# Kernel optimization log

Hardware: AMD Instinct MI355X
Metric: run time of the kernel (lower is better)

## Reference

```python
import jax, jax.numpy as jnp
import numpy as np

N_HEADS = 18
HEAD_DIM = 16
ROPE_THETA = 10000.0
SLIDING_WINDOW = 4096


def _rotate_half(x):
    half = x.shape[-1] // 2
    return jnp.concatenate([-x[..., half:], x[..., :half]], axis=-1)


def setup_inputs() -> dict:
    key = jax.random.key(0)
    k0, k1, k2, k3, k4 = jax.random.split(key, 5)
    B, S, H = 2, 2048, 288
    std = 0.02
    return {
        "hidden_states": jax.random.normal(k0, (B, S, H), dtype=jnp.float32),
        "Wq": jax.random.normal(k1, (H, H), dtype=jnp.float32) * std,
        "Wk": jax.random.normal(k2, (H, H), dtype=jnp.float32) * std,
        "Wv": jax.random.normal(k3, (H, H), dtype=jnp.float32) * std,
        "Wo": jax.random.normal(k4, (H, H), dtype=jnp.float32) * std,
    }


def reference(hidden_states, Wq, Wk, Wv, Wo):
    B, S, H = hidden_states.shape
    nH, D = N_HEADS, HEAD_DIM

    # QKV projections (nn.Linear: y = x @ W.T), reshape to [B, nH, S, D]
    def proj(W):
        return jnp.einsum("bsh,oh->bso", hidden_states, W).reshape(B, S, nH, D).transpose(0, 2, 1, 3)

    q, k, v = proj(Wq), proj(Wk), proj(Wv)

    # Rotary embedding: position_ids = arange(S)
    pos = jnp.arange(S, dtype=jnp.float32)
    inv_freq = 1.0 / (ROPE_THETA ** (jnp.arange(0, D, 2, dtype=jnp.float32) / D))
    freqs = pos[:, None] * inv_freq[None, :]            # [S, D/2]
    emb = jnp.concatenate([freqs, freqs], axis=-1)      # [S, D]
    cos = jnp.cos(emb)[None, None, :, :]                # [1, 1, S, D]
    sin = jnp.sin(emb)[None, None, :, :]
    q = q * cos + _rotate_half(q) * sin
    k = k * cos + _rotate_half(k) * sin

    # num_key_value_groups = 1 -> repeat_kv is identity.
    scores = jnp.einsum("bhqd,bhkd->bhqk", q, k) / jnp.sqrt(jnp.float32(D))

    # Sliding-window causal mask: attend iff 0 <= i - j < window
    i = jnp.arange(S)[:, None]
    j = jnp.arange(S)[None, :]
    allowed = (j <= i) & (i - j < SLIDING_WINDOW)       # [S, S]
    neg = jnp.finfo(scores.dtype).min
    scores = jnp.where(allowed[None, None, :, :], scores, neg)

    attn = jax.nn.softmax(scores.astype(jnp.float32), axis=-1).astype(q.dtype)
    out = jnp.einsum("bhqk,bhkd->bhqd", attn, v)        # [B, nH, S, D]
    out = out.transpose(0, 2, 1, 3).reshape(B, S, H)
    return jnp.einsum("bsh,oh->bso", out, Wo)
```

## Files before the change

kernel.cpp:

```cpp
#include <hip/hip_runtime.h>
#include <hip/hip_bf16.h>
#include <math.h>

#define H_DIM 288
#define NHEADS 18
#define HEAD_D 16
#define SEQ 2048
#define BATCH 2
#define M_TOT (BATCH*SEQ)
#define XCNT (M_TOT*H_DIM)
#define WCNT (H_DIM*H_DIM)
#define NUNITS 10368
#define NQUNITS 2304

typedef _Float16 f16_t;
typedef __attribute__((ext_vector_type(4))) _Float16 half4v;
typedef __attribute__((ext_vector_type(8))) _Float16 half8v;
typedef __attribute__((ext_vector_type(4))) float   float4v;

__global__ __launch_bounds__(256) void cvt_f16(
    const float* __restrict__ X,
    const float* __restrict__ Wq, const float* __restrict__ Wk,
    const float* __restrict__ Wv, const float* __restrict__ Wo,
    f16_t* __restrict__ Xf, f16_t* __restrict__ Wf)
{
    int idx = blockIdx.x * 256 + threadIdx.x;
    const int X4 = XCNT/4, W4 = WCNT/4;
    if (idx >= X4 + 4*W4) return;
    const float* src; f16_t* dst; int off;
    if (idx < X4) { src = X; dst = Xf; off = idx; }
    else {
        int r = idx - X4;
        int wz = r / W4; off = r - wz*W4;
        src = (wz==0) ? Wq : (wz==1) ? Wk : (wz==2) ? Wv : Wo;
        dst = Wf + (size_t)wz*WCNT;
    }
    float4 v = ((const float4*)src)[off];
    half4v h; h[0]=(f16_t)v.x; h[1]=(f16_t)v.y; h[2]=(f16_t)v.z; h[3]=(f16_t)v.w;
    ((half4v*)dst)[off] = h;
}

__global__ __launch_bounds__(64) void qkv_mfma(
    const f16_t* __restrict__ Xf, const f16_t* __restrict__ Wf,
    f16_t* __restrict__ Q16, f16_t* __restrict__ K16, f16_t* __restrict__ Vt)
{
    const int bx = blockIdx.x;
    const int z  = bx/6;
    const int n0 = (bx - z*6)*48;
    const int m0 = blockIdx.y*32;
    const int lane = threadIdx.x & 63;
    const int n = lane & 15, quad = lane >> 4;

    const f16_t* W = Wf + (size_t)z*WCNT;

    float4v acc[2][3];
    #pragma unroll
    for (int mt = 0; mt < 2; mt++)
        #pragma unroll
        for (int nt = 0; nt < 3; nt++)
            acc[mt][nt] = (float4v){0.f,0.f,0.f,0.f};

    for (int k0 = 0; k0 < H_DIM; k0 += 32) {
        half8v a[2], b[3];
        #pragma unroll
        for (int mt = 0; mt < 2; mt++)
            a[mt] = *(const half8v*)(Xf + (size_t)(m0 + mt*16 + n)*H_DIM + k0 + quad*8);
        #pragma unroll
        for (int nt = 0; nt < 3; nt++)
            b[nt] = *(const half8v*)(W + (size_t)(n0 + nt*16 + n)*H_DIM + k0 + quad*8);
        #pragma unroll
        for (int mt = 0; mt < 2; mt++)
            #pragma unroll
            for (int nt = 0; nt < 3; nt++)
                acc[mt][nt] = __builtin_amdgcn_mfma_f32_16x16x32_f16(a[mt], b[nt], acc[mt][nt], 0, 0, 0);
    }

    if (z < 2) {
        f16_t* dst = (z == 0) ? Q16 : K16;
        const float invf = exp2f(-1.6609640474436813f * (float)(n & 7));
        #pragma unroll
        for (int mt = 0; mt < 2; mt++) {
            #pragma unroll
            for (int r = 0; r < 4; r++) {
                int m = m0 + mt*16 + quad*4 + r;
                int bb = m >> 11, s = m & (SEQ - 1);
                float ang = (float)s * invf;
                float c, sn;
                sincosf(ang, &sn, &c);
                #pragma unroll
                for (int nt = 0; nt < 3; nt++) {
                    float own = acc[mt][nt][r];
                    float par = __shfl_xor(own, 8, 64);
                    float val = (n & 8) ? fmaf(own, c, par*sn) : fmaf(own, c, -par*sn);
                    if (z == 0) val *= 0.36067376022224085f;
                    int head = (n0 >> 4) + nt;
                    dst[((size_t)((bb*NHEADS + head)*SEQ) + s)*HEAD_D + n] = (f16_t)val;
                }
            }
        }
    } else {
        #pragma unroll
        for (int mt = 0; mt < 2; mt++)
            #pragma unroll
            for (int nt = 0; nt < 3; nt++)
                #pragma unroll
                for (int r = 0; r < 4; r++) {
                    int m = m0 + mt*16 + quad*4 + r;
                    int bb = m >> 11, s = m & (SEQ - 1);
                    int head = (n0 >> 4) + nt;
                    Vt[(size_t)(bb*NHEADS + head)*(SEQ*HEAD_D)
                       + (size_t)(s >> 4)*256 + n*16 + (s & 15)] = (f16_t)acc[mt][nt][r];
                }
    }
}

__global__ __launch_bounds__(256) void attn_part(
    const f16_t* __restrict__ Q16, const f16_t* __restrict__ K16,
    const f16_t* __restrict__ Vt,
    float4* __restrict__ accbuf, float* __restrict__ lbuf)
{
    const int unit = blockIdx.x*4 + (threadIdx.x >> 6);
    const int lane = threadIdx.x & 63;
    const int n = lane & 15, quad = lane >> 4;

    const int bh = unit / 288;
    const int rem = unit - bh*288;
    int g, t0;
    if      (rem < 8)   { g=0; t0=rem;     }
    else if (rem < 24)  { g=1; t0=rem-8;   }
    else if (rem < 48)  { g=2; t0=rem-24;  }
    else if (rem < 80)  { g=3; t0=rem-48;  }
    else if (rem < 120) { g=4; t0=rem-80;  }
    else if (rem < 168) { g=5; t0=rem-120; }
    else if (rem < 224) { g=6; t0=rem-168; }
    else                { g=7; t0=rem-224; }
    const int qd = t0 / (g+1);
    const int qp = 8*g + qd;
    const int chunk = t0 - qd*(g+1);
    const int q0 = qp*32;

    half4v qb0 = *(const half4v*)(Q16 + ((size_t)bh*SEQ + q0 + n)*HEAD_D + quad*4);
    half4v qb1 = *(const half4v*)(Q16 + ((size_t)bh*SEQ + q0 + 16 + n)*HEAD_D + quad*4);
    const f16_t* Kb = K16 + (size_t)bh * SEQ * HEAD_D;
    const f16_t* Vb = Vt  + (size_t)bh * SEQ * HEAD_D;

    const float4v zero = {0.f, 0.f, 0.f, 0.f};
    float4v acc0 = zero, acc1 = zero;
    float l0 = 0.f, l1 = 0.f;

    const int lim0 = 2*qp, lim1 = 2*qp + 1;
    const int ktlo = chunk*16;
    const int kthi = min(ktlo + 15, lim1);

    int kt = ktlo;
    half4v ka = *(const half4v*)(Kb + (size_t)(kt*16 + n)*HEAD_D + quad*4);
    half4v va = *(const half4v*)(Vb + (size_t)kt*256 + n*16 + quad*4);
    for (; kt <= kthi; kt++) {
        half4v kan, van;
        if (kt < kthi) {
            kan = *(const half4v*)(Kb + (size_t)((kt+1)*16 + n)*HEAD_D + quad*4);
            van = *(const half4v*)(Vb + (size_t)(kt+1)*256 + n*16 + quad*4);
        }
        {
            float4v s = __builtin_amdgcn_mfma_f32_16x16x16f16(ka, qb1, zero, 0, 0, 0);
            float p[4];
            #pragma unroll
            for (int r = 0; r < 4; r++) {
                float e = __builtin_amdgcn_exp2f(s[r]);
                p[r] = (kt == lim1 && quad*4 + r > n) ? 0.0f : e;
            }
            l1 += (p[0] + p[1]) + (p[2] + p[3]);
            half4v pb;
            pb[0]=(f16_t)p[0]; pb[1]=(f16_t)p[1]; pb[2]=(f16_t)p[2]; pb[3]=(f16_t)p[3];
            acc1 = __builtin_amdgcn_mfma_f32_16x16x16f16(va, pb, acc1, 0, 0, 0);
        }
        if (kt <= lim0) {
            float4v s = __builtin_amdgcn_mfma_f32_16x16x16f16(ka, qb0, zero, 0, 0, 0);
            float p[4];
            #pragma unroll
            for (int r = 0; r < 4; r++) {
                float e = __builtin_amdgcn_exp2f(s[r]);
                p[r] = (kt == lim0 && quad*4 + r > n) ? 0.0f : e;
            }
            l0 += (p[0] + p[1]) + (p[2] + p[3]);
            half4v pb;
            pb[0]=(f16_t)p[0]; pb[1]=(f16_t)p[1]; pb[2]=(f16_t)p[2]; pb[3]=(f16_t)p[3];
            acc0 = __builtin_amdgcn_mfma_f32_16x16x16f16(va, pb, acc0, 0, 0, 0);
        }
        ka = kan; va = van;
    }

    float4 a0; a0.x=acc0[0]; a0.y=acc0[1]; a0.z=acc0[2]; a0.w=acc0[3];
    float4 a1; a1.x=acc1[0]; a1.y=acc1[1]; a1.z=acc1[2]; a1.w=acc1[3];
    accbuf[((size_t)unit*2 + 0)*64 + lane] = a0;
    accbuf[((size_t)unit*2 + 1)*64 + lane] = a1;
    lbuf[((size_t)unit*2 + 0)*64 + lane] = l0;
    lbuf[((size_t)unit*2 + 1)*64 + lane] = l1;
}

__global__ __launch_bounds__(256) void attn_red(
    const float4* __restrict__ accbuf, const float* __restrict__ lbuf,
    f16_t* __restrict__ Of)
{
    const int wid = blockIdx.x*4 + (threadIdx.x >> 6);
    const int lane = threadIdx.x & 63;
    const int n = lane & 15, quad = lane >> 4;
    const int bh = wid >> 6, qp = wid & 63;
    const int b = bh / NHEADS, h = bh - b*NHEADS;
    const int g = qp >> 3, j = qp & 7;
    const int nch = g + 1;
    const int ubase = bh*288 + qp + 4*g*(g-1) + g*j;

    #pragma unroll
    for (int t = 0; t < 2; t++) {
        float4 a = {0.f, 0.f, 0.f, 0.f};
        float l = 0.f;
        for (int c = 0; c < nch; c++) {
            size_t idx = ((size_t)(ubase + c)*2 + t)*64 + lane;
            float4 v = accbuf[idx];
            a.x += v.x; a.y += v.y; a.z += v.z; a.w += v.w;
            l += lbuf[idx];
        }
        l += __shfl_xor(l, 16, 64);
        l += __shfl_xor(l, 32, 64);
        float inv = 1.0f / l;
        half4v o;
        o[0]=(f16_t)(a.x*inv); o[1]=(f16_t)(a.y*inv);
        o[2]=(f16_t)(a.z*inv); o[3]=(f16_t)(a.w*inv);
        *(half4v*)(Of + (size_t)(b*SEQ + qp*32 + t*16 + n)*H_DIM + h*HEAD_D + quad*4) = o;
    }
}

__global__ __launch_bounds__(64) void out_mfma(
    const f16_t* __restrict__ Of, const f16_t* __restrict__ Wo16,
    float* __restrict__ C)
{
    const int n0 = blockIdx.x * 48;
    const int m0 = blockIdx.y * 32;
    const int lane = threadIdx.x & 63;
    const int n = lane & 15, quad = lane >> 4;

    float4v acc[2][3];
    #pragma unroll
    for (int mt = 0; mt < 2; mt++)
        #pragma unroll
        for (int nt = 0; nt < 3; nt++)
            acc[mt][nt] = (float4v){0.f,0.f,0.f,0.f};

    for (int k0 = 0; k0 < H_DIM; k0 += 32) {
        half8v a[2], b[3];
        #pragma unroll
        for (int mt = 0; mt < 2; mt++)
            a[mt] = *(const half8v*)(Of + (size_t)(m0 + mt*16 + n)*H_DIM + k0 + quad*8);
        #pragma unroll
        for (int nt = 0; nt < 3; nt++)
            b[nt] = *(const half8v*)(Wo16 + (size_t)(n0 + nt*16 + n)*H_DIM + k0 + quad*8);
        #pragma unroll
        for (int mt = 0; mt < 2; mt++)
            #pragma unroll
            for (int nt = 0; nt < 3; nt++)
                acc[mt][nt] = __builtin_amdgcn_mfma_f32_16x16x32_f16(a[mt], b[nt], acc[mt][nt], 0, 0, 0);
    }
    #pragma unroll
    for (int mt = 0; mt < 2; mt++)
        #pragma unroll
        for (int nt = 0; nt < 3; nt++)
            #pragma unroll
            for (int r = 0; r < 4; r++) {
                int m = m0 + mt*16 + quad*4 + r;
                C[(size_t)m*H_DIM + n0 + nt*16 + n] = acc[mt][nt][r];
            }
}

extern "C" void kernel_launch(void* const* d_in, const int* in_sizes, int n_in,
                              void* d_out, int out_size, void* d_ws, size_t ws_size,
                              hipStream_t stream)
{
    const float* Xh = (const float*)d_in[0];
    const float* Wq = (const float*)d_in[1];
    const float* Wk = (const float*)d_in[2];
    const float* Wv = (const float*)d_in[3];
    const float* Wo = (const float*)d_in[4];
    float* out = (float*)d_out;

    f16_t* Xf  = (f16_t*)d_ws;
    f16_t* Wf  = Xf + XCNT;
    f16_t* Q16 = Wf + 4*(size_t)WCNT;
    f16_t* K16 = Q16 + XCNT;
    f16_t* Vt  = K16 + XCNT;
    f16_t* Of  = Vt + XCNT;
    float4* accbuf = (float4*)(Of + XCNT);
    float*  lbuf   = (float*)(accbuf + (size_t)NUNITS*2*64);

    const int total4 = (XCNT + 4*WCNT)/4;
    cvt_f16<<<dim3((total4 + 255)/256), 256, 0, stream>>>(Xh, Wq, Wk, Wv, Wo, Xf, Wf);
    qkv_mfma<<<dim3(18, 128), 64, 0, stream>>>(Xf, Wf, Q16, K16, Vt);
    attn_part<<<dim3(NUNITS/4), 256, 0, stream>>>(Q16, K16, Vt, accbuf, lbuf);
    attn_red<<<dim3(NQUNITS/4), 256, 0, stream>>>(accbuf, lbuf, Of);
    out_mfma<<<dim3(6, 128), 64, 0, stream>>>(Of, Wf + 3*(size_t)WCNT, out);
}
```

Before: 116.6 us.

## Fuse all five stages into one cooperative persistent kernel with grid syncs

Replaces the five separate launches (convert, QKV GEMM, partial attention, reduction, output GEMM) with a single cooperative kernel of 512 blocks that loops over each stage's work units and separates stages with grid.sync(). This is meant to remove per-launch overhead and inter-kernel gaps. It also adds a fully unrolled fast path for unmasked 16-tile attention chunks that preloads all K/V fragments before computing. In exchange it relies on cooperative launch residency, adds grid-wide barrier cost, and raises register pressure under launch_bounds(256,2).

```diff
diff --git a/kernel.cpp b/kernel.cpp
--- a/kernel.cpp
+++ b/kernel.cpp
@@ -1,6 +1,9 @@
 #include <hip/hip_runtime.h>
 #include <hip/hip_bf16.h>
+#include <hip/hip_cooperative_groups.h>
 #include <math.h>
+
+namespace cg = cooperative_groups;
 
 #define H_DIM 288
 #define NHEADS 18
@@ -12,264 +15,287 @@
 #define WCNT (H_DIM*H_DIM)
 #define NUNITS 10368
 #define NQUNITS 2304
+#define NBLK 512
+#define NGW (NBLK*4)
 
 typedef _Float16 f16_t;
 typedef __attribute__((ext_vector_type(4))) _Float16 half4v;
 typedef __attribute__((ext_vector_type(8))) _Float16 half8v;
 typedef __attribute__((ext_vector_type(4))) float   float4v;
 
-__global__ __launch_bounds__(256) void cvt_f16(
+__global__ __launch_bounds__(256, 2) void fused_attn(
     const float* __restrict__ X,
     const float* __restrict__ Wq, const float* __restrict__ Wk,
     const float* __restrict__ Wv, const float* __restrict__ Wo,
-    f16_t* __restrict__ Xf, f16_t* __restrict__ Wf)
+    float* __restrict__ out,
+    f16_t* __restrict__ Xf, f16_t* __restrict__ Wf,
+    f16_t* __restrict__ Q16, f16_t* __restrict__ K16, f16_t* __restrict__ Vt,
+    f16_t* __restrict__ Of, float4* __restrict__ accbuf, float* __restrict__ lbuf)
 {
-    int idx = blockIdx.x * 256 + threadIdx.x;
-    const int X4 = XCNT/4, W4 = WCNT/4;
-    if (idx >= X4 + 4*W4) return;
-    const float* src; f16_t* dst; int off;
-    if (idx < X4) { src = X; dst = Xf; off = idx; }
-    else {
-        int r = idx - X4;
-        int wz = r / W4; off = r - wz*W4;
-        src = (wz==0) ? Wq : (wz==1) ? Wk : (wz==2) ? Wv : Wo;
-        dst = Wf + (size_t)wz*WCNT;
-    }
-    float4 v = ((const float4*)src)[off];
-    half4v h; h[0]=(f16_t)v.x; h[1]=(f16_t)v.y; h[2]=(f16_t)v.z; h[3]=(f16_t)v.w;
-    ((half4v*)dst)[off] = h;
-}
-
-__global__ __launch_bounds__(64) void qkv_mfma(
-    const f16_t* __restrict__ Xf, const f16_t* __restrict__ Wf,
-    f16_t* __restrict__ Q16, f16_t* __restrict__ K16, f16_t* __restrict__ Vt)
-{
-    const int bx = blockIdx.x;
-    const int z  = bx/6;
-    const int n0 = (bx - z*6)*48;
-    const int m0 = blockIdx.y*32;
+    cg::grid_group grid = cg::this_grid();
+    const int wave = threadIdx.x >> 6;
     const int lane = threadIdx.x & 63;
     const int n = lane & 15, quad = lane >> 4;
-
-    const f16_t* W = Wf + (size_t)z*WCNT;
-
-    float4v acc[2][3];
-    #pragma unroll
-    for (int mt = 0; mt < 2; mt++)
-        #pragma unroll
-        for (int nt = 0; nt < 3; nt++)
-            acc[mt][nt] = (float4v){0.f,0.f,0.f,0.f};
-
-    for (int k0 = 0; k0 < H_DIM; k0 += 32) {
-        half8v a[2], b[3];
+    const int gwave = blockIdx.x*4 + wave;
+
+    {
+        const int tid = blockIdx.x*256 + threadIdx.x;
+        const int X4 = XCNT/4, W4 = WCNT/4;
+        const int total4 = X4 + 4*W4;
+        for (int i = tid; i < total4; i += NBLK*256) {
+            const float* src; f16_t* dst; int off;
+            if (i < X4) { src = X; dst = Xf; off = i; }
+            else {
+                int r = i - X4;
+                int wz = r / W4; off = r - wz*W4;
+                src = (wz==0) ? Wq : (wz==1) ? Wk : (wz==2) ? Wv : Wo;
+                dst = Wf + (size_t)wz*WCNT;
+            }
+            float4 v = ((const float4*)src)[off];
+            half4v h; h[0]=(f16_t)v.x; h[1]=(f16_t)v.y; h[2]=(f16_t)v.z; h[3]=(f16_t)v.w;
+            ((half4v*)dst)[off] = h;
+        }
+    }
+    grid.sync();
+
+    for (int u = gwave; u < 2304; u += NGW) {
+        const int bx = u % 18;
+        const int by = u / 18;
+        const int z  = bx/6;
+        const int n0 = (bx - z*6)*48;
+        const int m0 = by*32;
+        const f16_t* W = Wf + (size_t)z*WCNT;
+
+        float4v acc[2][3];
         #pragma unroll
         for (int mt = 0; mt < 2; mt++)
-            a[mt] = *(const half8v*)(Xf + (size_t)(m0 + mt*16 + n)*H_DIM + k0 + quad*8);
-        #pragma unroll
-        for (int nt = 0; nt < 3; nt++)
-            b[nt] = *(const half8v*)(W + (size_t)(n0 + nt*16 + n)*H_DIM + k0 + quad*8);
-        #pragma unroll
-        for (int mt = 0; mt < 2; mt++)
-            #pragma unroll
-            for (int nt = 0; nt < 3; nt++)
-                acc[mt][nt] = __builtin_amdgcn_mfma_f32_16x16x32_f16(a[mt], b[nt], acc[mt][nt], 0, 0, 0);
-    }
-
-    if (z < 2) {
-        f16_t* dst = (z == 0) ? Q16 : K16;
-        const float invf = exp2f(-1.6609640474436813f * (float)(n & 7));
-        #pragma unroll
-        for (int mt = 0; mt < 2; mt++) {
-            #pragma unroll
-            for (int r = 0; r < 4; r++) {
-                int m = m0 + mt*16 + quad*4 + r;
-                int bb = m >> 11, s = m & (SEQ - 1);
-                float ang = (float)s * invf;
-                float c, sn;
-                sincosf(ang, &sn, &c);
-                #pragma unroll
-                for (int nt = 0; nt < 3; nt++) {
-                    float own = acc[mt][nt][r];
-                    float par = __shfl_xor(own, 8, 64);
-                    float val = (n & 8) ? fmaf(own, c, par*sn) : fmaf(own, c, -par*sn);
-                    if (z == 0) val *= 0.36067376022224085f;
-                    int head = (n0 >> 4) + nt;
-                    dst[((size_t)((bb*NHEADS + head)*SEQ) + s)*HEAD_D + n] = (f16_t)val;
-                }
-            }
-        }
-    } else {
-        #pragma unroll
-        for (int mt = 0; mt < 2; mt++)
-            #pragma unroll
-            for (int nt = 0; nt < 3; nt++)
+            #pragma unroll
+            for (int nt = 0; nt < 3; nt++)
+                acc[mt][nt] = (float4v){0.f,0.f,0.f,0.f};
+
+        for (int k0 = 0; k0 < H_DIM; k0 += 32) {
+            half8v a[2], b[3];
+            #pragma unroll
+            for (int mt = 0; mt < 2; mt++)
+                a[mt] = *(const half8v*)(Xf + (size_t)(m0 + mt*16 + n)*H_DIM + k0 + quad*8);
+            #pragma unroll
+            for (int nt = 0; nt < 3; nt++)
+                b[nt] = *(const half8v*)(W + (size_t)(n0 + nt*16 + n)*H_DIM + k0 + quad*8);
+            #pragma unroll
+            for (int mt = 0; mt < 2; mt++)
+                #pragma unroll
+                for (int nt = 0; nt < 3; nt++)
+                    acc[mt][nt] = __builtin_amdgcn_mfma_f32_16x16x32_f16(a[mt], b[nt], acc[mt][nt], 0, 0, 0);
+        }
+
+        if (z < 2) {
+            f16_t* dst = (z == 0) ? Q16 : K16;
+            const float invf = exp2f(-1.6609640474436813f * (float)(n & 7));
+            #pragma unroll
+            for (int mt = 0; mt < 2; mt++) {
                 #pragma unroll
                 for (int r = 0; r < 4; r++) {
                     int m = m0 + mt*16 + quad*4 + r;
                     int bb = m >> 11, s = m & (SEQ - 1);
-                    int head = (n0 >> 4) + nt;
-                    Vt[(size_t)(bb*NHEADS + head)*(SEQ*HEAD_D)
-                       + (size_t)(s >> 4)*256 + n*16 + (s & 15)] = (f16_t)acc[mt][nt][r];
-                }
-    }
-}
-
-__global__ __launch_bounds__(256) void attn_part(
-    const f16_t* __restrict__ Q16, const f16_t* __restrict__ K16,
-    const f16_t* __restrict__ Vt,
-    float4* __restrict__ accbuf, float* __restrict__ lbuf)
-{
-    const int unit = blockIdx.x*4 + (threadIdx.x >> 6);
-    const int lane = threadIdx.x & 63;
-    const int n = lane & 15, quad = lane >> 4;
-
-    const int bh = unit / 288;
-    const int rem = unit - bh*288;
-    int g, t0;
-    if      (rem < 8)   { g=0; t0=rem;     }
-    else if (rem < 24)  { g=1; t0=rem-8;   }
-    else if (rem < 48)  { g=2; t0=rem-24;  }
-    else if (rem < 80)  { g=3; t0=rem-48;  }
-    else if (rem < 120) { g=4; t0=rem-80;  }
-    else if (rem < 168) { g=5; t0=rem-120; }
-    else if (rem < 224) { g=6; t0=rem-168; }
-    else                { g=7; t0=rem-224; }
-    const int qd = t0 / (g+1);
-    const int qp = 8*g + qd;
-    const int chunk = t0 - qd*(g+1);
-    const int q0 = qp*32;
-
-    half4v qb0 = *(const half4v*)(Q16 + ((size_t)bh*SEQ + q0 + n)*HEAD_D + quad*4);
-    half4v qb1 = *(const half4v*)(Q16 + ((size_t)bh*SEQ + q0 + 16 + n)*HEAD_D + quad*4);
-    const f16_t* Kb = K16 + (size_t)bh * SEQ * HEAD_D;
-    const f16_t* Vb = Vt  + (size_t)bh * SEQ * HEAD_D;
-
-    const float4v zero = {0.f, 0.f, 0.f, 0.f};
-    float4v acc0 = zero, acc1 = zero;
-    float l0 = 0.f, l1 = 0.f;
-
-    const int lim0 = 2*qp, lim1 = 2*qp + 1;
-    const int ktlo = chunk*16;
-    const int kthi = min(ktlo + 15, lim1);
-
-    int kt = ktlo;
-    half4v ka = *(const half4v*)(Kb + (size_t)(kt*16 + n)*HEAD_D + quad*4);
-    half4v va = *(const half4v*)(Vb + (size_t)kt*256 + n*16 + quad*4);
-    for (; kt <= kthi; kt++) {
-        half4v kan, van;
-        if (kt < kthi) {
-            kan = *(const half4v*)(Kb + (size_t)((kt+1)*16 + n)*HEAD_D + quad*4);
-            van = *(const half4v*)(Vb + (size_t)(kt+1)*256 + n*16 + quad*4);
-        }
-        {
-            float4v s = __builtin_amdgcn_mfma_f32_16x16x16f16(ka, qb1, zero, 0, 0, 0);
-            float p[4];
-            #pragma unroll
-            for (int r = 0; r < 4; r++) {
-                float e = __builtin_amdgcn_exp2f(s[r]);
-                p[r] = (kt == lim1 && quad*4 + r > n) ? 0.0f : e;
-            }
-            l1 += (p[0] + p[1]) + (p[2] + p[3]);
-            half4v pb;
-            pb[0]=(f16_t)p[0]; pb[1]=(f16_t)p[1]; pb[2]=(f16_t)p[2]; pb[3]=(f16_t)p[3];
-            acc1 = __builtin_amdgcn_mfma_f32_16x16x16f16(va, pb, acc1, 0, 0, 0);
-        }
-        if (kt <= lim0) {
-            float4v s = __builtin_amdgcn_mfma_f32_16x16x16f16(ka, qb0, zero, 0, 0, 0);
-            float p[4];
-            #pragma unroll
-            for (int r = 0; r < 4; r++) {
-                float e = __builtin_amdgcn_exp2f(s[r]);
-                p[r] = (kt == lim0 && quad*4 + r > n) ? 0.0f : e;
-            }
-            l0 += (p[0] + p[1]) + (p[2] + p[3]);
-            half4v pb;
-            pb[0]=(f16_t)p[0]; pb[1]=(f16_t)p[1]; pb[2]=(f16_t)p[2]; pb[3]=(f16_t)p[3];
-            acc0 = __builtin_amdgcn_mfma_f32_16x16x16f16(va, pb, acc0, 0, 0, 0);
-        }
-        ka = kan; va = van;
-    }
-
-    float4 a0; a0.x=acc0[0]; a0.y=acc0[1]; a0.z=acc0[2]; a0.w=acc0[3];
-    float4 a1; a1.x=acc1[0]; a1.y=acc1[1]; a1.z=acc1[2]; a1.w=acc1[3];
-    accbuf[((size_t)unit*2 + 0)*64 + lane] = a0;
-    accbuf[((size_t)unit*2 + 1)*64 + lane] = a1;
-    lbuf[((size_t)unit*2 + 0)*64 + lane] = l0;
-    lbuf[((size_t)unit*2 + 1)*64 + lane] = l1;
-}
-
-__global__ __launch_bounds__(256) void attn_red(
-    const float4* __restrict__ accbuf, const float* __restrict__ lbuf,
-    f16_t* __restrict__ Of)
-{
-    const int wid = blockIdx.x*4 + (threadIdx.x >> 6);
-    const int lane = threadIdx.x & 63;
-    const int n = lane & 15, quad = lane >> 4;
-    const int bh = wid >> 6, qp = wid & 63;
-    const int b = bh / NHEADS, h = bh - b*NHEADS;
-    const int g = qp >> 3, j = qp & 7;
-    const int nch = g + 1;
-    const int ubase = bh*288 + qp + 4*g*(g-1) + g*j;
-
-    #pragma unroll
-    for (int t = 0; t < 2; t++) {
-        float4 a = {0.f, 0.f, 0.f, 0.f};
-        float l = 0.f;
-        for (int c = 0; c < nch; c++) {
-            size_t idx = ((size_t)(ubase + c)*2 + t)*64 + lane;
-            float4 v = accbuf[idx];
-            a.x += v.x; a.y += v.y; a.z += v.z; a.w += v.w;
-            l += lbuf[idx];
-        }
-        l += __shfl_xor(l, 16, 64);
-        l += __shfl_xor(l, 32, 64);
-        float inv = 1.0f / l;
-        half4v o;
-        o[0]=(f16_t)(a.x*inv); o[1]=(f16_t)(a.y*inv);
-        o[2]=(f16_t)(a.z*inv); o[3]=(f16_t)(a.w*inv);
-        *(half4v*)(Of + (size_t)(b*SEQ + qp*32 + t*16 + n)*H_DIM + h*HEAD_D + quad*4) = o;
-    }
-}
-
-__global__ __launch_bounds__(64) void out_mfma(
-    const f16_t* __restrict__ Of, const f16_t* __restrict__ Wo16,
-    float* __restrict__ C)
-{
-    const int n0 = blockIdx.x * 48;
-    const int m0 = blockIdx.y * 32;
-    const int lane = threadIdx.x & 63;
-    const int n = lane & 15, quad = lane >> 4;
-
-    float4v acc[2][3];
-    #pragma unroll
-    for (int mt = 0; mt < 2; mt++)
+                    float ang = (float)s * invf;
+                    float c, sn;
+                    sincosf(ang, &sn, &c);
+                    #pragma unroll
+                    for (int nt = 0; nt < 3; nt++) {
+                        float own = acc[mt][nt][r];
+                        float par = __shfl_xor(own, 8, 64);
+                        float val = (n & 8) ? fmaf(own, c, par*sn) : fmaf(own, c, -par*sn);
+                        if (z == 0) val *= 0.36067376022224085f;
+                        int head = (n0 >> 4) + nt;
+                        dst[((size_t)((bb*NHEADS + head)*SEQ) + s)*HEAD_D + n] = (f16_t)val;
+                    }
+                }
+            }
+        } else {
+            #pragma unroll
+            for (int mt = 0; mt < 2; mt++)
+                #pragma unroll
+                for (int nt = 0; nt < 3; nt++)
+                    #pragma unroll
+                    for (int r = 0; r < 4; r++) {
+                        int m = m0 + mt*16 + quad*4 + r;
+                        int bb = m >> 11, s = m & (SEQ - 1);
+                        int head = (n0 >> 4) + nt;
+                        Vt[(size_t)(bb*NHEADS + head)*(SEQ*HEAD_D)
+                           + (size_t)(s >> 4)*256 + n*16 + (s & 15)] = (f16_t)acc[mt][nt][r];
+                    }
+        }
+    }
+    grid.sync();
+
+    for (int unit = gwave; unit < NUNITS; unit += NGW) {
+        const int bh = unit / 288;
+        const int rem = unit - bh*288;
+        int g, t0;
+        if      (rem < 8)   { g=0; t0=rem;     }
+        else if (rem < 24)  { g=1; t0=rem-8;   }
+        else if (rem < 48)  { g=2; t0=rem-24;  }
+        else if (rem < 80)  { g=3; t0=rem-48;  }
+        else if (rem < 120) { g=4; t0=rem-80;  }
+        else if (rem < 168) { g=5; t0=rem-120; }
+        else if (rem < 224) { g=6; t0=rem-168; }
+        else                { g=7; t0=rem-224; }
+        const int qd = t0 / (g+1);
+        const int qp = 8*g + qd;
+        const int chunk = t0 - qd*(g+1);
+        const int q0 = qp*32;
+
+        half4v qb0 = *(const half4v*)(Q16 + ((size_t)bh*SEQ + q0 + n)*HEAD_D + quad*4);
+        half4v qb1 = *(const half4v*)(Q16 + ((size_t)bh*SEQ + q0 + 16 + n)*HEAD_D + quad*4);
+        const f16_t* Kb = K16 + (size_t)bh * SEQ * HEAD_D;
+        const f16_t* Vb = Vt  + (size_t)bh * SEQ * HEAD_D;
+        const int loff = n*16 + quad*4;
+
+        const float4v zero = {0.f, 0.f, 0.f, 0.f};
+        float4v acc0 = zero, acc1 = zero;
+        float l0 = 0.f, l1 = 0.f;
+
+        const int lim0 = 2*qp, lim1 = 2*qp + 1;
+        const int ktlo = chunk*16;
+        const int kthi = min(ktlo + 15, lim1);
+
+        if (ktlo + 15 < lim0) {
+            half4v KA[16], VA[16];
+            #pragma unroll
+            for (int i = 0; i < 16; i++) {
+                KA[i] = *(const half4v*)(Kb + (size_t)(ktlo + i)*256 + loff);
+                VA[i] = *(const half4v*)(Vb + (size_t)(ktlo + i)*256 + loff);
+            }
+            #pragma unroll
+            for (int i = 0; i < 16; i++) {
+                float4v s1 = __builtin_amdgcn_mfma_f32_16x16x16f16(KA[i], qb1, zero, 0, 0, 0);
+                float4v s0 = __builtin_amdgcn_mfma_f32_16x16x16f16(KA[i], qb0, zero, 0, 0, 0);
+                float p1[4], p0[4];
+                #pragma unroll
+                for (int r = 0; r < 4; r++) { p1[r] = __builtin_amdgcn_exp2f(s1[r]); p0[r] = __builtin_amdgcn_exp2f(s0[r]); }
+                l1 += (p1[0]+p1[1]) + (p1[2]+p1[3]);
+                l0 += (p0[0]+p0[1]) + (p0[2]+p0[3]);
+                half4v pb1, pb0;
+                #pragma unroll
+                for (int r = 0; r < 4; r++) { pb1[r]=(f16_t)p1[r]; pb0[r]=(f16_t)p0[r]; }
+                acc1 = __builtin_amdgcn_mfma_f32_16x16x16f16(VA[i], pb1, acc1, 0, 0, 0);
+                acc0 = __builtin_amdgcn_mfma_f32_16x16x16f16(VA[i], pb0, acc0, 0, 0, 0);
+            }
+        } else {
+            int kt = ktlo;
+            half4v ka = *(const half4v*)(Kb + (size_t)kt*256 + loff);
+            half4v va = *(const half4v*)(Vb + (size_t)kt*256 + loff);
+            for (; kt <= kthi; kt++) {
+                half4v kan, van;
+                if (kt < kthi) {
+                    kan = *(const half4v*)(Kb + (size_t)(kt+1)*256 + loff);
+                    van = *(const half4v*)(Vb + (size_t)(kt+1)*256 + loff);
+                }
+                {
+                    float4v s = __builtin_amdgcn_mfma_f32_16x16x16f16(ka, qb1, zero, 0, 0, 0);
+                    float p[4];
+                    #pragma unroll
+                    for (int r = 0; r < 4; r++) {
+                        float e = __builtin_amdgcn_exp2f(s[r]);
+                        p[r] = (kt == lim1 && quad*4 + r > n) ? 0.0f : e;
+                    }
+                    l1 += (p[0]+p[1]) + (p[2]+p[3]);
+                    half4v pb;
+                    #pragma unroll
+                    for (int r = 0; r < 4; r++) pb[r]=(f16_t)p[r];
+                    acc1 = __builtin_amdgcn_mfma_f32_16x16x16f16(va, pb, acc1, 0, 0, 0);
+                }
+                if (kt <= lim0) {
+                    float4v s = __builtin_amdgcn_mfma_f32_16x16x16f16(ka, qb0, zero, 0, 0, 0);
+                    float p[4];
+                    #pragma unroll
+                    for (int r = 0; r < 4; r++) {
+                        float e = __builtin_amdgcn_exp2f(s[r]);
+                        p[r] = (kt == lim0 && quad*4 + r > n) ? 0.0f : e;
+                    }
+                    l0 += (p[0]+p[1]) + (p[2]+p[3]);
+                    half4v pb;
+                    #pragma unroll
+                    for (int r = 0; r < 4; r++) pb[r]=(f16_t)p[r];
+                    acc0 = __builtin_amdgcn_mfma_f32_16x16x16f16(va, pb, acc0, 0, 0, 0);
+                }
+                ka = kan; va = van;
+            }
+        }
+
+        float4 a0; a0.x=acc0[0]; a0.y=acc0[1]; a0.z=acc0[2]; a0.w=acc0[3];
+        float4 a1; a1.x=acc1[0]; a1.y=acc1[1]; a1.z=acc1[2]; a1.w=acc1[3];
+        accbuf[((size_t)unit*2 + 0)*64 + lane] = a0;
+        accbuf[((size_t)unit*2 + 1)*64 + lane] = a1;
+        lbuf[((size_t)unit*2 + 0)*64 + lane] = l0;
+        lbuf[((size_t)unit*2 + 1)*64 + lane] = l1;
+    }
+    grid.sync();
+
+    for (int wid = gwave; wid < NQUNITS; wid += NGW) {
+        const int bh = wid >> 6, qp = wid & 63;
+        const int b = bh / NHEADS, h = bh - b*NHEADS;
+        const int g = qp >> 3, j = qp & 7;
+        const int nch = g + 1;
+        const int ubase = bh*288 + qp + 4*g*(g-1) + g*j;
+
         #pragma unroll
-        for (int nt = 0; nt < 3; nt++)
-            acc[mt][nt] = (float4v){0.f,0.f,0.f,0.f};
-
-    for (int k0 = 0; k0 < H_DIM; k0 += 32) {
-        half8v a[2], b[3];
+        for (int t = 0; t < 2; t++) {
+            float4 a = {0.f, 0.f, 0.f, 0.f};
+            float l = 0.f;
+            for (int c = 0; c < nch; c++) {
+                size_t idx = ((size_t)(ubase + c)*2 + t)*64 + lane;
+                float4 v = accbuf[idx];
+                a.x += v.x; a.y += v.y; a.z += v.z; a.w += v.w;
+                l += lbuf[idx];
+            }
+            l += __shfl_xor(l, 16, 64);
+            l += __shfl_xor(l, 32, 64);
+            float inv = 1.0f / l;
+            half4v o;
+            o[0]=(f16_t)(a.x*inv); o[1]=(f16_t)(a.y*inv);
+            o[2]=(f16_t)(a.z*inv); o[3]=(f16_t)(a.w*inv);
+            *(half4v*)(Of + (size_t)(b*SEQ + qp*32 + t*16 + n)*H_DIM + h*HEAD_D + quad*4) = o;
+        }
+    }
+    grid.sync();
+
+    for (int u = gwave; u < 768; u += NGW) {
+        const int n0 = (u % 6) * 48;
+        const int m0 = (u / 6) * 32;
+        const f16_t* Wo16 = Wf + 3*(size_t)WCNT;
+
+        float4v acc[2][3];
         #pragma unroll
         for (int mt = 0; mt < 2; mt++)
-            a[mt] = *(const half8v*)(Of + (size_t)(m0 + mt*16 + n)*H_DIM + k0 + quad*8);
-        #pragma unroll
-        for (int nt = 0; nt < 3; nt++)
-            b[nt] = *(const half8v*)(Wo16 + (size_t)(n0 + nt*16 + n)*H_DIM + k0 + quad*8);
+            #pragma unroll
+            for (int nt = 0; nt < 3; nt++)
+                acc[mt][nt] = (float4v){0.f,0.f,0.f,0.f};
+
+        for (int k0 = 0; k0 < H_DIM; k0 += 32) {
+            half8v a[2], b[3];
+            #pragma unroll
+            for (int mt = 0; mt < 2; mt++)
+                a[mt] = *(const half8v*)(Of + (size_t)(m0 + mt*16 + n)*H_DIM + k0 + quad*8);
+            #pragma unroll
+            for (int nt = 0; nt < 3; nt++)
+                b[nt] = *(const half8v*)(Wo16 + (size_t)(n0 + nt*16 + n)*H_DIM + k0 + quad*8);
+            #pragma unroll
+            for (int mt = 0; mt < 2; mt++)
+                #pragma unroll
+                for (int nt = 0; nt < 3; nt++)
+                    acc[mt][nt] = __builtin_amdgcn_mfma_f32_16x16x32_f16(a[mt], b[nt], acc[mt][nt], 0, 0, 0);
+        }
         #pragma unroll
         for (int mt = 0; mt < 2; mt++)
             #pragma unroll
             for (int nt = 0; nt < 3; nt++)
-                acc[mt][nt] = __builtin_amdgcn_mfma_f32_16x16x32_f16(a[mt], b[nt], acc[mt][nt], 0, 0, 0);
-    }
-    #pragma unroll
-    for (int mt = 0; mt < 2; mt++)
-        #pragma unroll
-        for (int nt = 0; nt < 3; nt++)
-            #pragma unroll
-            for (int r = 0; r < 4; r++) {
-                int m = m0 + mt*16 + quad*4 + r;
-                C[(size_t)m*H_DIM + n0 + nt*16 + n] = acc[mt][nt][r];
-            }
+                #pragma unroll
+                for (int r = 0; r < 4; r++) {
+                    int m = m0 + mt*16 + quad*4 + r;
+                    out[(size_t)m*H_DIM + n0 + nt*16 + n] = acc[mt][nt][r];
+                }
+    }
 }
 
 extern "C" void kernel_launch(void* const* d_in, const int* in_sizes, int n_in,
@@ -292,10 +318,11 @@
     float4* accbuf = (float4*)(Of + XCNT);
     float*  lbuf   = (float*)(accbuf + (size_t)NUNITS*2*64);
 
-    const int total4 = (XCNT + 4*WCNT)/4;
-    cvt_f16<<<dim3((total4 + 255)/256), 256, 0, stream>>>(Xh, Wq, Wk, Wv, Wo, Xf, Wf);
-    qkv_mfma<<<dim3(18, 128), 64, 0, stream>>>(Xf, Wf, Q16, K16, Vt);
-    attn_part<<<dim3(NUNITS/4), 256, 0, stream>>>(Q16, K16, Vt, accbuf, lbuf);
-    attn_red<<<dim3(NQUNITS/4), 256, 0, stream>>>(accbuf, lbuf, Of);
-    out_mfma<<<dim3(6, 128), 64, 0, stream>>>(Of, Wf + 3*(size_t)WCNT, out);
+    void* args[] = {
+        (void*)&Xh, (void*)&Wq, (void*)&Wk, (void*)&Wv, (void*)&Wo,
+        (void*)&out, (void*)&Xf, (void*)&Wf, (void*)&Q16, (void*)&K16,
+        (void*)&Vt, (void*)&Of, (void*)&accbuf, (void*)&lbuf
+    };
+    hipLaunchCooperativeKernel((const void*)fused_attn, dim3(NBLK), dim3(256),
+                               args, 0, stream);
 }
```

New measurement: 374.5 us. +221.2%, slower.

## Add unmasked fully-unrolled attention fast path, packed f16 conversion, and hardware sin/cos RoPE

Applied to the files above, without the earlier changes.

Attention chunks that lie entirely below the causal diagonal now take a fast path. It loads all 16 K/V tiles up front, then runs a fully unrolled loop with no mask checks or per-iteration branches. This exposes more memory-level parallelism and interleaves the two query tiles' MFMAs. Probability packing now uses cvt_pkrtz, which rounds toward zero. RoPE sin/cos uses the hardware sin/cos instructions on an input range-reduced to revolutions. The trade-offs are higher register pressure from the 32 preloaded half4 vectors, slightly different rounding, and lower trig accuracy for large angles.

```diff
diff --git a/kernel.cpp b/kernel.cpp
--- a/kernel.cpp
+++ b/kernel.cpp
@@ -14,6 +14,7 @@
 #define NQUNITS 2304
 
 typedef _Float16 f16_t;
+typedef __attribute__((ext_vector_type(2))) _Float16 half2v;
 typedef __attribute__((ext_vector_type(4))) _Float16 half4v;
 typedef __attribute__((ext_vector_type(8))) _Float16 half8v;
 typedef __attribute__((ext_vector_type(4))) float   float4v;
@@ -77,16 +78,18 @@
 
     if (z < 2) {
         f16_t* dst = (z == 0) ? Q16 : K16;
-        const float invf = exp2f(-1.6609640474436813f * (float)(n & 7));
+        const float invf_rev = exp2f(-1.6609640474436813f * (float)(n & 7))
+                             * 0.15915494309189535f;
         #pragma unroll
         for (int mt = 0; mt < 2; mt++) {
             #pragma unroll
             for (int r = 0; r < 4; r++) {
                 int m = m0 + mt*16 + quad*4 + r;
                 int bb = m >> 11, s = m & (SEQ - 1);
-                float ang = (float)s * invf;
-                float c, sn;
-                sincosf(ang, &sn, &c);
+                float rev = (float)s * invf_rev;
+                float fr = rev - floorf(rev);
+                float sn = __builtin_amdgcn_sinf(fr);
+                float c  = __builtin_amdgcn_cosf(fr);
                 #pragma unroll
                 for (int nt = 0; nt < 3; nt++) {
                     float own = acc[mt][nt][r];
@@ -112,6 +115,13 @@
                        + (size_t)(s >> 4)*256 + n*16 + (s & 15)] = (f16_t)acc[mt][nt][r];
                 }
     }
+}
+
+__device__ __forceinline__ half4v pack4(const float p[4]) {
+    half2v ab = __builtin_bit_cast(half2v, __builtin_amdgcn_cvt_pkrtz(p[0], p[1]));
+    half2v cd = __builtin_bit_cast(half2v, __builtin_amdgcn_cvt_pkrtz(p[2], p[3]));
+    half4v o; o[0]=ab[0]; o[1]=ab[1]; o[2]=cd[0]; o[3]=cd[1];
+    return o;
 }
 
 __global__ __launch_bounds__(256) void attn_part(
@@ -143,6 +153,7 @@
     half4v qb1 = *(const half4v*)(Q16 + ((size_t)bh*SEQ + q0 + 16 + n)*HEAD_D + quad*4);
     const f16_t* Kb = K16 + (size_t)bh * SEQ * HEAD_D;
     const f16_t* Vb = Vt  + (size_t)bh * SEQ * HEAD_D;
+    const int loff = n*16 + quad*4;
 
     const float4v zero = {0.f, 0.f, 0.f, 0.f};
     float4v acc0 = zero, acc1 = zero;
@@ -152,42 +163,59 @@
     const int ktlo = chunk*16;
     const int kthi = min(ktlo + 15, lim1);
 
-    int kt = ktlo;
-    half4v ka = *(const half4v*)(Kb + (size_t)(kt*16 + n)*HEAD_D + quad*4);
-    half4v va = *(const half4v*)(Vb + (size_t)kt*256 + n*16 + quad*4);
-    for (; kt <= kthi; kt++) {
-        half4v kan, van;
-        if (kt < kthi) {
-            kan = *(const half4v*)(Kb + (size_t)((kt+1)*16 + n)*HEAD_D + quad*4);
-            van = *(const half4v*)(Vb + (size_t)(kt+1)*256 + n*16 + quad*4);
-        }
-        {
-            float4v s = __builtin_amdgcn_mfma_f32_16x16x16f16(ka, qb1, zero, 0, 0, 0);
-            float p[4];
-            #pragma unroll
-            for (int r = 0; r < 4; r++) {
-                float e = __builtin_amdgcn_exp2f(s[r]);
-                p[r] = (kt == lim1 && quad*4 + r > n) ? 0.0f : e;
-            }
-            l1 += (p[0] + p[1]) + (p[2] + p[3]);
-            half4v pb;
-            pb[0]=(f16_t)p[0]; pb[1]=(f16_t)p[1]; pb[2]=(f16_t)p[2]; pb[3]=(f16_t)p[3];
-            acc1 = __builtin_amdgcn_mfma_f32_16x16x16f16(va, pb, acc1, 0, 0, 0);
-        }
-        if (kt <= lim0) {
-            float4v s = __builtin_amdgcn_mfma_f32_16x16x16f16(ka, qb0, zero, 0, 0, 0);
-            float p[4];
-            #pragma unroll
-            for (int r = 0; r < 4; r++) {
-                float e = __builtin_amdgcn_exp2f(s[r]);
-                p[r] = (kt == lim0 && quad*4 + r > n) ? 0.0f : e;
-            }
-            l0 += (p[0] + p[1]) + (p[2] + p[3]);
-            half4v pb;
-            pb[0]=(f16_t)p[0]; pb[1]=(f16_t)p[1]; pb[2]=(f16_t)p[2]; pb[3]=(f16_t)p[3];
-            acc0 = __builtin_amdgcn_mfma_f32_16x16x16f16(va, pb, acc0, 0, 0, 0);
-        }
-        ka = kan; va = van;
+    if (ktlo + 15 < lim0) {
+        half4v KA[16], VA[16];
+        #pragma unroll
+        for (int i = 0; i < 16; i++) {
+            KA[i] = *(const half4v*)(Kb + (size_t)(ktlo + i)*256 + loff);
+            VA[i] = *(const half4v*)(Vb + (size_t)(ktlo + i)*256 + loff);
+        }
+        #pragma unroll
+        for (int i = 0; i < 16; i++) {
+            float4v s1 = __builtin_amdgcn_mfma_f32_16x16x16f16(KA[i], qb1, zero, 0, 0, 0);
+            float4v s0 = __builtin_amdgcn_mfma_f32_16x16x16f16(KA[i], qb0, zero, 0, 0, 0);
+            float p1[4], p0[4];
+            #pragma unroll
+            for (int r = 0; r < 4; r++) { p1[r] = __builtin_amdgcn_exp2f(s1[r]); p0[r] = __builtin_amdgcn_exp2f(s0[r]); }
+            l1 += (p1[0]+p1[1]) + (p1[2]+p1[3]);
+            l0 += (p0[0]+p0[1]) + (p0[2]+p0[3]);
+            acc1 = __builtin_amdgcn_mfma_f32_16x16x16f16(VA[i], pack4(p1), acc1, 0, 0, 0);
+            acc0 = __builtin_amdgcn_mfma_f32_16x16x16f16(VA[i], pack4(p0), acc0, 0, 0, 0);
+        }
+    } else {
+        int kt = ktlo;
+        half4v ka = *(const half4v*)(Kb + (size_t)kt*256 + loff);
+        half4v va = *(const half4v*)(Vb + (size_t)kt*256 + loff);
+        for (; kt <= kthi; kt++) {
+            half4v kan, van;
+            if (kt < kthi) {
+                kan = *(const half4v*)(Kb + (size_t)(kt+1)*256 + loff);
+                van = *(const half4v*)(Vb + (size_t)(kt+1)*256 + loff);
+            }
+            {
+                float4v s = __builtin_amdgcn_mfma_f32_16x16x16f16(ka, qb1, zero, 0, 0, 0);
+                float p[4];
+                #pragma unroll
+                for (int r = 0; r < 4; r++) {
+                    float e = __builtin_amdgcn_exp2f(s[r]);
+                    p[r] = (kt == lim1 && quad*4 + r > n) ? 0.0f : e;
+                }
+                l1 += (p[0]+p[1]) + (p[2]+p[3]);
+                acc1 = __builtin_amdgcn_mfma_f32_16x16x16f16(va, pack4(p), acc1, 0, 0, 0);
+            }
+            if (kt <= lim0) {
+                float4v s = __builtin_amdgcn_mfma_f32_16x16x16f16(ka, qb0, zero, 0, 0, 0);
+                float p[4];
+                #pragma unroll
+                for (int r = 0; r < 4; r++) {
+                    float e = __builtin_amdgcn_exp2f(s[r]);
+                    p[r] = (kt == lim0 && quad*4 + r > n) ? 0.0f : e;
+                }
+                l0 += (p[0]+p[1]) + (p[2]+p[3]);
+                acc0 = __builtin_amdgcn_mfma_f32_16x16x16f16(va, pack4(p), acc0, 0, 0, 0);
+            }
+            ka = kan; va = van;
+        }
     }
 
     float4 a0; a0.x=acc0[0]; a0.y=acc0[1]; a0.z=acc0[2]; a0.w=acc0[3];
```

After: 112.6 us, median of 2. 3.5% less time.
